# Optimization experiments

Hardware: AMD Instinct MI355X
Metric: run time of the kernel (lower is better)

## Reference

```python
import jax, jax.numpy as jnp
import numpy as np

B, L, D, N_ITEMS = 512, 128, 512, 50000


def setup_inputs() -> dict:
    key = jax.random.key(0)
    ks = jax.random.split(key, 12)
    s = 1.0 / np.sqrt(D)
    x = jax.random.randint(ks[0], (B, L), 0, N_ITEMS)
    # cumulative event times (strictly increasing per sequence)
    t = jnp.cumsum(jax.random.uniform(ks[1], (B, L), dtype=jnp.float32), axis=1)
    # embedding table, xavier-ish, padding_idx=0 row zeroed
    emb = (jax.random.normal(ks[2], (N_ITEMS, D), dtype=jnp.float32) * s).at[0].set(0.0)
    # GRUCell params (torch layout: gates ordered r, z, n)
    W_ih = jax.random.uniform(ks[3], (3 * D, D), minval=-s, maxval=s, dtype=jnp.float32)
    W_hh = jax.random.uniform(ks[4], (3 * D, D), minval=-s, maxval=s, dtype=jnp.float32)
    b_ih = jax.random.uniform(ks[5], (3 * D,), minval=-s, maxval=s, dtype=jnp.float32)
    b_hh = jax.random.uniform(ks[6], (3 * D,), minval=-s, maxval=s, dtype=jnp.float32)
    # ODEFunc: 2-layer MLP f(h) = W2 @ tanh(W1 @ h + b1) + b2
    W1 = jax.random.normal(ks[7], (D, D), dtype=jnp.float32) * s
    b1 = jnp.zeros((D,), jnp.float32)
    W2 = jax.random.normal(ks[8], (D, D), dtype=jnp.float32) * s
    b2 = jnp.zeros((D,), jnp.float32)
    return dict(t=t, emb=emb, W_ih=W_ih, W_hh=W_hh, b_ih=b_ih, b_hh=b_hh,
                W1=W1, b1=b1, W2=W2, b2=b2, x=x)


def reference(t, emb, W_ih, W_hh, b_ih, b_hh, W1, b1, W2, b2, x):
    dtype = emb.dtype
    x_emb = emb[x]  # [B, L, D]
    # inter-event deltas, dt[:,0] = 0
    dt = jnp.concatenate([jnp.zeros_like(t[:, :1]), t[:, 1:] - t[:, :-1]], axis=1)
    mask = (x != 0).astype(dtype)[..., None]  # [B, L, 1]

    def f(h):  # ODE dynamics (autonomous MLP)
        return jnp.tanh(h @ W1.T + b1) @ W2.T + b2

    def rk4(h, dt_):  # dt_ : [B, 1]
        k1 = f(h)
        k2 = f(h + 0.5 * dt_ * k1)
        k3 = f(h + 0.5 * dt_ * k2)
        k4 = f(h + dt_ * k3)
        return h + (dt_ / 6.0) * (k1 + 2.0 * k2 + 2.0 * k3 + k4)

    def gru_cell(xi, h):  # torch GRUCell math, gate order r,z,n
        gi = xi @ W_ih.T + b_ih
        gh = h @ W_hh.T + b_hh
        ir, iz, inn = jnp.split(gi, 3, axis=-1)
        hr, hz, hn = jnp.split(gh, 3, axis=-1)
        r = jax.nn.sigmoid(ir + hr)
        z = jax.nn.sigmoid(iz + hz)
        n = jnp.tanh(inn + r * hn)
        return (1.0 - z) * n + z * h

    xs = (jnp.swapaxes(x_emb, 0, 1),            # [L, B, D]
          jnp.swapaxes(dt, 0, 1)[..., None],    # [L, B, 1]
          jnp.swapaxes(mask, 0, 1),             # [L, B, 1]
          jnp.arange(t.shape[1]))               # step index

    def step(h, inp):
        xi, dti, mi, i = inp
        dti_c = jnp.maximum(dti, 1e-6)
        h_ev = rk4(h, dti_c)
        h = jnp.where(i > 0, h_ev * mi + h * (1.0 - mi), h)
        h_new = gru_cell(xi, h)
        h = h_new * mi + h * (1.0 - mi)
        return h, None

    h0 = jnp.zeros((t.shape[0], emb.shape[1]), dtype)
    h, _ = jax.lax.scan(step, h0, xs)
    return h  # [B, D]
```

## Files before the change

kernel.cpp:

```cpp
#include <hip/hip_runtime.h>

#define L_SEQ 128
#define BATCH 512
#define DIM   512

typedef __attribute__((ext_vector_type(8))) short bf16x8;
typedef __attribute__((ext_vector_type(4))) float f32x4;
typedef unsigned short ushort_t;

#define MFMA16(a,b,c) __builtin_amdgcn_mfma_f32_16x16x32_bf16((a),(b),(c),0,0,0)

__device__ __forceinline__ ushort_t f2bf(float f) {
  union { float f; unsigned u; } v; v.f = f;
  unsigned u = v.u;
  unsigned r = (u + 0x7FFFu + ((u >> 16) & 1u)) >> 16;
  return (ushort_t)r;
}
__device__ __forceinline__ float bf2f(ushort_t b) {
  union { unsigned u; float f; } v; v.u = ((unsigned)b) << 16;
  return v.f;
}
__device__ __forceinline__ int aoff(int r, int k) {
  return (r << 10) + ((((k >> 3) ^ (r & 7)) << 4) | ((k & 7) << 1));
}
__device__ __forceinline__ float tanh_f(float x) {
  x = fminf(fmaxf(x, -15.f), 15.f);
  float e = __expf(2.f * x);
  return (e - 1.f) / (e + 1.f);
}
__device__ __forceinline__ float sigm_f(float x) {
  x = fminf(fmaxf(x, -30.f), 30.f);
  return 1.f / (1.f + __expf(-x));
}


__global__ __launch_bounds__(256) void prep_w(const float* __restrict__ W1,
                                              const float* __restrict__ W2,
                                              const float* __restrict__ Whh,
                                              const float* __restrict__ Wih,
                                              ushort_t* __restrict__ wsb) {
  unsigned idx = blockIdx.x * 256u + threadIdx.x;
  unsigned m  = idx >> 18;
  unsigned r  = idx & 262143u;
  unsigned s  = r >> 14;
  unsigned r1 = r & 16383u;
  unsigned w  = r1 >> 10;
  unsigned r2 = r1 & 1023u;
  unsigned g  = r2 >> 8;
  unsigned r3 = r2 & 255u;
  unsigned cc = r3 >> 3;
  unsigned j  = r3 & 7u;
  unsigned c  = w * 32u + cc;
  unsigned k  = s * 32u + g * 8u + j;
  float v;
  if (m == 0)      v = W1[c * 512u + k];
  else if (m == 1) v = W2[c * 512u + k];
  else if (m < 5)  v = Whh[((m - 2u) * 512u + c) * 512u + k];
  else             v = Wih[((m - 5u) * 512u + c) * 512u + k];
  wsb[idx] = f2bf(v);
}

__global__ __launch_bounds__(256) void gi_gemm(const float* __restrict__ emb,
                                               const int* __restrict__ x,
                                               const float* __restrict__ bih,
                                               const ushort_t* __restrict__ wsb,
                                               ushort_t* __restrict__ gib) {
  __shared__ __align__(16) unsigned char As[64 * 1024];
  const int tid = threadIdx.x;
  const int mb = blockIdx.x;
  const int nb = blockIdx.y;
  const int i = (mb * 64) >> 9;
  const int brow0 = (mb * 64) & 511;
  {
    int r = tid >> 2;
    int xv = x[(brow0 + r) * L_SEQ + i];
    const float4* er4 = (const float4*)(emb + (size_t)xv * DIM);
#pragma unroll
    for (int cc = 0; cc < 16; ++cc) {
      int c = (tid & 3) * 16 + cc;
      float4 fa = er4[c * 2], fb = er4[c * 2 + 1];
      union { ushort_t u[8]; bf16x8 v; } pk;
      pk.u[0] = f2bf(fa.x); pk.u[1] = f2bf(fa.y); pk.u[2] = f2bf(fa.z); pk.u[3] = f2bf(fa.w);
      pk.u[4] = f2bf(fb.x); pk.u[5] = f2bf(fb.y); pk.u[6] = f2bf(fb.z); pk.u[7] = f2bf(fb.w);
      *(bf16x8*)(As + aoff(r, c * 8)) = pk.v;
    }
  }
  __syncthreads();
  const int wave = tid >> 6, lane = tid & 63;
  const int lr = lane & 15, lg = lane >> 4;
  const int ncol0 = nb * 256 + wave * 64;
  const int gate = nb >> 1;
  const ushort_t* wimg = wsb + (5u + (unsigned)gate) * 262144u;
  int bofs[4];
#pragma unroll
  for (int nf = 0; nf < 4; ++nf) {
    int cg = (nb & 1) * 256 + wave * 64 + nf * 16 + lr;
    bofs[nf] = (cg >> 5) * 1024 + (cg & 31) * 8 + lg * 256;
  }
  f32x4 acc[4][4];
  f32x4 z = {0.f, 0.f, 0.f, 0.f};
#pragma unroll
  for (int mf = 0; mf < 4; ++mf)
#pragma unroll
    for (int nf = 0; nf < 4; ++nf) acc[mf][nf] = z;
#pragma unroll
  for (int kf = 0; kf < 16; ++kf) {
    bf16x8 a[4];
#pragma unroll
    for (int mf = 0; mf < 4; ++mf)
      a[mf] = *(const bf16x8*)(As + aoff((mf << 4) + lr, (kf << 5) + (lg << 3)));
#pragma unroll
    for (int nf = 0; nf < 4; ++nf) {
      bf16x8 b = *(const bf16x8*)(wimg + kf * 16384 + bofs[nf]);
#pragma unroll
      for (int mf = 0; mf < 4; ++mf) acc[mf][nf] = MFMA16(a[mf], b, acc[mf][nf]);
    }
  }
#pragma unroll
  for (int nf = 0; nf < 4; ++nf) {
    int col = ncol0 + (nf << 4) + lr;
    float bb = bih[col];
#pragma unroll
    for (int mf = 0; mf < 4; ++mf)
#pragma unroll
      for (int j = 0; j < 4; ++j) {
        int row = (mf << 4) + (lg << 2) + j;
        __builtin_nontemporal_store(f2bf(acc[mf][nf][j] + bb),
            gib + (size_t)(i * BATCH + brow0 + row) * 1536 + col);
      }
  }
}


__device__ __forceinline__ void barrier_nd() {
  asm volatile("s_waitcnt lgkmcnt(0)" ::: "memory");
  __builtin_amdgcn_s_barrier();
}

__device__ __forceinline__ void dma_slice(const ushort_t* __restrict__ wsb,
                                          int ip, int ij, int wave, int lane,
                                          unsigned char* dst) {
  unsigned moff = (ip < 8) ? ((unsigned)(ip & 1) << 18) : ((unsigned)(ip - 6) << 18);
  const ushort_t* src = wsb + moff + ((unsigned)ij << 14) + ((unsigned)wave << 10) + ((unsigned)lane << 3);
  __builtin_amdgcn_global_load_lds((const __attribute__((address_space(1))) unsigned int*)src,
                                   (__attribute__((address_space(3))) unsigned int*)dst, 16, 0, 0);
  __builtin_amdgcn_global_load_lds((const __attribute__((address_space(1))) unsigned int*)(src + 512),
                                   (__attribute__((address_space(3))) unsigned int*)(dst + 1024), 16, 0, 0);
}

__device__ __forceinline__ void phase_mm(const unsigned char* __restrict__ Aimg,
                                         unsigned char* __restrict__ wbw,
                                         const ushort_t* __restrict__ wsb,
                                         int wave, int lane,
                                         int& cslot, int& ip, int& ij, f32x4 acc[2]) {
  const int lr = lane & 15, lg = lane >> 4;
  f32x4 z = {0.f, 0.f, 0.f, 0.f};
  acc[0] = z; acc[1] = z;
#pragma unroll 2
  for (int kf = 0; kf < 16; ++kf) {
    asm volatile("s_waitcnt vmcnt(4)" ::: "memory");
    __builtin_amdgcn_sched_barrier(0);
    unsigned char* wb = wbw + cslot * 2048;
    bf16x8 a = *(const bf16x8*)(Aimg + (lr << 10) + ((((kf << 2) + lg) ^ (lr & 7)) << 4));
    bf16x8 p = *(const bf16x8*)(wb + (lg << 9) + (lr << 4));
    bf16x8 q = *(const bf16x8*)(wb + (lg << 9) + 256 + (lr << 4));
    asm volatile("s_waitcnt lgkmcnt(0)" ::: "memory");
    __builtin_amdgcn_sched_barrier(0);
    dma_slice(wsb, ip, ij, wave, lane, wb);
    if (++ij == 16) { ij = 0; if (++ip == 11) ip = 0; }
    cslot = (cslot == 2) ? 0 : cslot + 1;
    acc[0] = MFMA16(a, p, acc[0]);
    acc[1] = MFMA16(a, q, acc[1]);
  }
}

__global__ __launch_bounds__(1024, 4) void scan_kernel(
    const float* __restrict__ t, const int* __restrict__ x,
    const ushort_t* __restrict__ wsb,
    const float* __restrict__ b1g, const float* __restrict__ b2g,
    const float* __restrict__ bhhg,
    const ushort_t* __restrict__ gib, float* __restrict__ out) {
  extern __shared__ unsigned char smem[];
  unsigned char* WBUF = smem;
  unsigned char* S0   = smem + 98304;
  unsigned char* S1   = smem + 114688;
  float* b1s  = (float*)(smem + 131072);
  float* b2s  = (float*)(smem + 133120);
  float* bhhs = (float*)(smem + 135168);

  const int tid = threadIdx.x;
  const int wave = tid >> 6, lane = tid & 63;
  const int lr = lane & 15, lg = lane >> 4;
  const int n0 = wave * 32;
  const int b0 = blockIdx.x * 16;
  unsigned char* wbw = WBUF + wave * 6144;

  for (int q = tid; q < 512; q += 1024) { b1s[q] = b1g[q]; b2s[q] = b2g[q]; }
  for (int q = tid; q < 1536; q += 1024) bhhs[q] = bhhg[q];
  { bf16x8 zz = {0, 0, 0, 0, 0, 0, 0, 0}; *(bf16x8*)(S0 + tid * 16) = zz; }
  __syncthreads();

  float dtj[4], mj[4];
#pragma unroll
  for (int j = 0; j < 4; ++j) {
    int b = b0 + lg * 4 + j;
    mj[j] = (x[b * L_SEQ + 0] != 0) ? 1.f : 0.f;
    dtj[j] = 1e-6f;
  }
  ushort_t gv[3][2][4];
#pragma unroll
  for (int nf = 0; nf < 2; ++nf)
#pragma unroll
    for (int j = 0; j < 4; ++j) {
      const ushort_t* gp = gib + (size_t)(b0 + lg * 4 + j) * 1536 + n0 + nf * 16 + lr;
      gv[0][nf][j] = __builtin_nontemporal_load(gp);
      gv[1][nf][j] = __builtin_nontemporal_load(gp + 512);
      gv[2][nf][j] = __builtin_nontemporal_load(gp + 1024);
    }

  int cslot = 0, ip = 8, ij = 0;
#pragma unroll
  for (int k = 0; k < 3; ++k) { dma_slice(wsb, ip, ij, wave, lane, wbw + k * 2048); ++ij; }

  float h[2][4];
#pragma unroll
  for (int nf = 0; nf < 2; ++nf)
#pragma unroll
    for (int j = 0; j < 4; ++j) h[nf][j] = 0.f;

  for (int i = 0; i < L_SEQ; ++i) {
    barrier_nd();

    if (i > 0) {
      float ksum[2][4] = {};
      for (int s = 0; s < 4; ++s) {
        f32x4 a1[2];
        phase_mm(S0, wbw, wsb, wave, lane, cslot, ip, ij, a1);
#pragma unroll
        for (int nf = 0; nf < 2; ++nf) {
          int col = n0 + nf * 16 + lr;
          float bb = b1s[col];
#pragma unroll
          for (int j = 0; j < 4; ++j)
            *(ushort_t*)(S1 + aoff(lg * 4 + j, col)) = f2bf(tanh_f(a1[nf][j] + bb));
        }
        barrier_nd();
        f32x4 a2[2];
        phase_mm(S1, wbw, wsb, wave, lane, cslot, ip, ij, a2);
        const float wk = (s == 0 || s == 3) ? 1.f : 2.f;
        const float cs = (s < 2) ? 0.5f : 1.f;
#pragma unroll
        for (int nf = 0; nf < 2; ++nf) {
          int col = n0 + nf * 16 + lr;
          float bb = b2s[col];
#pragma unroll
          for (int j = 0; j < 4; ++j) {
            float kv = a2[nf][j] + bb;
            ksum[nf][j] += wk * kv;
            float nv;
            if (s < 3) {
              nv = h[nf][j] + cs * dtj[j] * kv;
            } else {
              float hev = h[nf][j] + dtj[j] * (1.f / 6.f) * ksum[nf][j];
              nv = (mj[j] > 0.5f) ? hev : h[nf][j];
              h[nf][j] = nv;
            }
            *(ushort_t*)(S0 + aoff(lg * 4 + j, col)) = f2bf(nv);
          }
        }
        barrier_nd();
      }
    }

    f32x4 gh0[2], gh1[2], gh2[2];
    phase_mm(S0, wbw, wsb, wave, lane, cslot, ip, ij, gh0);
    phase_mm(S0, wbw, wsb, wave, lane, cslot, ip, ij, gh1);
    phase_mm(S0, wbw, wsb, wave, lane, cslot, ip, ij, gh2);
    barrier_nd();

    int in_ = (i < L_SEQ - 1) ? i + 1 : i;
    float dtn[4], mn[4];
#pragma unroll
    for (int j = 0; j < 4; ++j) {
      int b = b0 + lg * 4 + j;
      mn[j] = (x[b * L_SEQ + in_] != 0) ? 1.f : 0.f;
      dtn[j] = fmaxf(t[b * L_SEQ + in_] - t[b * L_SEQ + in_ - 1], 1e-6f);
    }
    ushort_t gvn[3][2][4];
#pragma unroll
    for (int nf = 0; nf < 2; ++nf)
#pragma unroll
      for (int j = 0; j < 4; ++j) {
        const ushort_t* gp = gib + (size_t)(in_ * BATCH + b0 + lg * 4 + j) * 1536 + n0 + nf * 16 + lr;
        gvn[0][nf][j] = __builtin_nontemporal_load(gp);
        gvn[1][nf][j] = __builtin_nontemporal_load(gp + 512);
        gvn[2][nf][j] = __builtin_nontemporal_load(gp + 1024);
      }

#pragma unroll
    for (int nf = 0; nf < 2; ++nf) {
      int col = n0 + nf * 16 + lr;
      float br = bhhs[col], bz = bhhs[col + 512], bn = bhhs[col + 1024];
#pragma unroll
      for (int j = 0; j < 4; ++j) {
        float rr = sigm_f(bf2f(gv[0][nf][j]) + gh0[nf][j] + br);
        float zz = sigm_f(bf2f(gv[1][nf][j]) + gh1[nf][j] + bz);
        float nn = tanh_f(bf2f(gv[2][nf][j]) + rr * (gh2[nf][j] + bn));
        float hnew = (1.f - zz) * nn + zz * h[nf][j];
        float hv = (mj[j] > 0.5f) ? hnew : h[nf][j];
        h[nf][j] = hv;
        *(ushort_t*)(S0 + aoff(lg * 4 + j, col)) = f2bf(hv);
      }
    }
#pragma unroll
    for (int j = 0; j < 4; ++j) { dtj[j] = dtn[j]; mj[j] = mn[j]; }
#pragma unroll
    for (int g = 0; g < 3; ++g)
#pragma unroll
      for (int nf = 0; nf < 2; ++nf)
#pragma unroll
        for (int j = 0; j < 4; ++j) gv[g][nf][j] = gvn[g][nf][j];
  }

  asm volatile("s_waitcnt vmcnt(0)" ::: "memory");
#pragma unroll
  for (int nf = 0; nf < 2; ++nf) {
    int col = n0 + nf * 16 + lr;
#pragma unroll
    for (int j = 0; j < 4; ++j) {
      int b = b0 + lg * 4 + j;
      out[(size_t)b * DIM + col] = h[nf][j];
    }
  }
}

extern "C" void kernel_launch(void* const* d_in, const int* in_sizes, int n_in,
                              void* d_out, int out_size, void* d_ws, size_t ws_size,
                              hipStream_t stream) {
  const float* t_   = (const float*)d_in[0];
  const float* emb  = (const float*)d_in[1];
  const float* Wih  = (const float*)d_in[2];
  const float* Whh  = (const float*)d_in[3];
  const float* bih  = (const float*)d_in[4];
  const float* bhh  = (const float*)d_in[5];
  const float* W1   = (const float*)d_in[6];
  const float* b1   = (const float*)d_in[7];
  const float* W2   = (const float*)d_in[8];
  const float* b2   = (const float*)d_in[9];
  const int*   x    = (const int*)d_in[10];
  float* out = (float*)d_out;
  (void)b2; (void)in_sizes; (void)n_in; (void)out_size; (void)ws_size;

  ushort_t* wsb = (ushort_t*)d_ws;
  ushort_t* gib = wsb + 2097152;

  (void)hipFuncSetAttribute((const void*)scan_kernel,
                            hipFuncAttributeMaxDynamicSharedMemorySize, 141312);

  hipLaunchKernelGGL(prep_w, dim3(8192), dim3(256), 0, stream, W1, W2, Whh, Wih, wsb);
  hipLaunchKernelGGL(gi_gemm, dim3(1024, 6), dim3(256), 0, stream, emb, x, bih, wsb, gib);
  hipLaunchKernelGGL(scan_kernel, dim3(32), dim3(1024), 141312, stream,
                     t_, x, wsb, b1, b2, bhh, gib, out);
}
```

Baseline: 7.696 ms.

## Split each batch group across two blocks exchanging hidden halves via global flags

The scan kernel now runs 64 blocks of 512 threads instead of 32 blocks of 1024. Each pair of blocks owns one batch group and computes half of the output columns each. At every matmul phase the two blocks swap their halves of the activation through global memory, guarded by atomic flag counters and spin-waits, and the final output buffer serves as the exchange scratch. Weights are streamed straight into registers with inline-asm global loads instead of the LDS DMA ring, and the weight image is re-laid out in column halves. The aim is to put twice as many CUs on the latency-bound recurrence, at the cost of a cross-block handshake on every phase.

```diff
diff --git a/kernel.cpp b/kernel.cpp
--- a/kernel.cpp
+++ b/kernel.cpp
@@ -31,6 +31,10 @@
 __device__ __forceinline__ float sigm_f(float x) {
   x = fminf(fmaxf(x, -30.f), 30.f);
   return 1.f / (1.f + __expf(-x));
+}
+__device__ __forceinline__ void barrier_nd() {
+  asm volatile("s_waitcnt lgkmcnt(0)" ::: "memory");
+  __builtin_amdgcn_s_barrier();
 }
 
 
@@ -42,15 +46,16 @@
   unsigned idx = blockIdx.x * 256u + threadIdx.x;
   unsigned m  = idx >> 18;
   unsigned r  = idx & 262143u;
-  unsigned s  = r >> 14;
-  unsigned r1 = r & 16383u;
+  unsigned hf = r >> 17;  r &= 131071u;
+  unsigned s  = r >> 13;
+  unsigned r1 = r & 8191u;
   unsigned w  = r1 >> 10;
   unsigned r2 = r1 & 1023u;
   unsigned g  = r2 >> 8;
   unsigned r3 = r2 & 255u;
   unsigned cc = r3 >> 3;
   unsigned j  = r3 & 7u;
-  unsigned c  = w * 32u + cc;
+  unsigned c  = hf * 256u + w * 32u + cc;
   unsigned k  = s * 32u + g * 8u + j;
   float v;
   if (m == 0)      v = W1[c * 512u + k];
@@ -95,7 +100,8 @@
 #pragma unroll
   for (int nf = 0; nf < 4; ++nf) {
     int cg = (nb & 1) * 256 + wave * 64 + nf * 16 + lr;
-    bofs[nf] = (cg >> 5) * 1024 + (cg & 31) * 8 + lg * 256;
+    int hfc = cg >> 8, chw = cg & 255;
+    bofs[nf] = hfc * 131072 + (chw >> 5) * 1024 + (chw & 31) * 8 + lg * 256;
   }
   f32x4 acc[4][4];
   f32x4 z = {0.f, 0.f, 0.f, 0.f};
@@ -111,7 +117,7 @@
       a[mf] = *(const bf16x8*)(As + aoff((mf << 4) + lr, (kf << 5) + (lg << 3)));
 #pragma unroll
     for (int nf = 0; nf < 4; ++nf) {
-      bf16x8 b = *(const bf16x8*)(wimg + kf * 16384 + bofs[nf]);
+      bf16x8 b = *(const bf16x8*)(wimg + kf * 8192 + bofs[nf]);
 #pragma unroll
       for (int mf = 0; mf < 4; ++mf) acc[mf][nf] = MFMA16(a[mf], b, acc[mf][nf]);
     }
@@ -132,73 +138,100 @@
 }
 
 
-__device__ __forceinline__ void barrier_nd() {
-  asm volatile("s_waitcnt lgkmcnt(0)" ::: "memory");
-  __builtin_amdgcn_s_barrier();
-}
-
-__device__ __forceinline__ void dma_slice(const ushort_t* __restrict__ wsb,
-                                          int ip, int ij, int wave, int lane,
-                                          unsigned char* dst) {
-  unsigned moff = (ip < 8) ? ((unsigned)(ip & 1) << 18) : ((unsigned)(ip - 6) << 18);
-  const ushort_t* src = wsb + moff + ((unsigned)ij << 14) + ((unsigned)wave << 10) + ((unsigned)lane << 3);
-  __builtin_amdgcn_global_load_lds((const __attribute__((address_space(1))) unsigned int*)src,
-                                   (__attribute__((address_space(3))) unsigned int*)dst, 16, 0, 0);
-  __builtin_amdgcn_global_load_lds((const __attribute__((address_space(1))) unsigned int*)(src + 512),
-                                   (__attribute__((address_space(3))) unsigned int*)(dst + 1024), 16, 0, 0);
-}
-
-__device__ __forceinline__ void phase_mm(const unsigned char* __restrict__ Aimg,
-                                         unsigned char* __restrict__ wbw,
-                                         const ushort_t* __restrict__ wsb,
-                                         int wave, int lane,
-                                         int& cslot, int& ip, int& ij, f32x4 acc[2]) {
-  const int lr = lane & 15, lg = lane >> 4;
-  f32x4 z = {0.f, 0.f, 0.f, 0.f};
-  acc[0] = z; acc[1] = z;
-#pragma unroll 2
-  for (int kf = 0; kf < 16; ++kf) {
-    asm volatile("s_waitcnt vmcnt(4)" ::: "memory");
-    __builtin_amdgcn_sched_barrier(0);
-    unsigned char* wb = wbw + cslot * 2048;
-    bf16x8 a = *(const bf16x8*)(Aimg + (lr << 10) + ((((kf << 2) + lg) ^ (lr & 7)) << 4));
-    bf16x8 p = *(const bf16x8*)(wb + (lg << 9) + (lr << 4));
-    bf16x8 q = *(const bf16x8*)(wb + (lg << 9) + 256 + (lr << 4));
-    asm volatile("s_waitcnt lgkmcnt(0)" ::: "memory");
-    __builtin_amdgcn_sched_barrier(0);
-    dma_slice(wsb, ip, ij, wave, lane, wb);
-    if (++ij == 16) { ij = 0; if (++ip == 11) ip = 0; }
-    cslot = (cslot == 2) ? 0 : cslot + 1;
-    acc[0] = MFMA16(a, p, acc[0]);
-    acc[1] = MFMA16(a, q, acc[1]);
-  }
-}
-
-__global__ __launch_bounds__(1024, 4) void scan_kernel(
+#define ISSUE16(BASE) do { \
+    _Pragma("unroll") \
+    for (int q_ = 0; q_ < 16; ++q_) { \
+      int s_ = (q_ < 8) ? (sb0 + q_) : (sb1 + q_ - 8); \
+      const ushort_t* a_ = (BASE) + (unsigned)s_ * 8192u; \
+      asm volatile("global_load_dwordx4 %0, %2, off\n\t" \
+                   "global_load_dwordx4 %1, %2, off offset:256" \
+                   : "=&v"(Rr[q_][0]), "=&v"(Rr[q_][1]) : "v"(a_) : "memory"); \
+    } } while (0)
+
+#define CONS1(IMG, Q, SS, VM) do { \
+    asm volatile("s_waitcnt vmcnt(" #VM ")" ::: "memory"); \
+    __builtin_amdgcn_sched_barrier(0); \
+    bf16x8 a_ = *(const bf16x8*)((IMG) + (lr << 10) + ((((SS) * 4 + lg) ^ (lr & 7)) << 4)); \
+    acc[0] = MFMA16(a_, Rr[Q][0], acc[0]); \
+    acc[1] = MFMA16(a_, Rr[Q][1], acc[1]); } while (0)
+
+#define CONS_LO(IMG) do { CONS1(IMG,0,sb0+0,30); CONS1(IMG,1,sb0+1,28); \
+    CONS1(IMG,2,sb0+2,26); CONS1(IMG,3,sb0+3,24); CONS1(IMG,4,sb0+4,22); \
+    CONS1(IMG,5,sb0+5,20); CONS1(IMG,6,sb0+6,18); CONS1(IMG,7,sb0+7,16); } while (0)
+#define CONS_HI(IMG) do { CONS1(IMG,8,sb1+0,14); CONS1(IMG,9,sb1+1,12); \
+    CONS1(IMG,10,sb1+2,10); CONS1(IMG,11,sb1+3,8); CONS1(IMG,12,sb1+4,6); \
+    CONS1(IMG,13,sb1+5,4); CONS1(IMG,14,sb1+6,2); CONS1(IMG,15,sb1+7,0); } while (0)
+
+#define HEAD() do { \
+    asm volatile("" :: "v"(o0), "v"(o1)); \
+    asm volatile("s_waitcnt vmcnt(0)" ::: "memory"); \
+    __syncthreads(); \
+    if (tid == 0) (void)__hip_atomic_fetch_add(myflag, 1u, __ATOMIC_RELAXED, __HIP_MEMORY_SCOPE_AGENT); \
+  } while (0)
+
+#define EXPORT(IMG) do { \
+    int row_ = tid >> 5, ch_ = tid & 31; \
+    union { unsigned long long u[2]; bf16x8 v; } pk_; \
+    pk_.v = *(const bf16x8*)((IMG) + (row_ << 10) + (((hf * 32 + ch_) ^ (row_ & 7)) << 4)); \
+    unsigned long long* d_ = xb + ((size_t)((g * 2 + (int)(pc & 1u)) * 2 + hf) * 1024) + tid * 2; \
+    o0 = __hip_atomic_exchange(d_,     pk_.u[0], __ATOMIC_RELAXED, __HIP_MEMORY_SCOPE_AGENT); \
+    o1 = __hip_atomic_exchange(d_ + 1, pk_.u[1], __ATOMIC_RELAXED, __HIP_MEMORY_SCOPE_AGENT); \
+  } while (0)
+
+#define IMPORT(IMG) do { \
+    if (tid == 0) { unsigned tgt_ = pc + 1u; \
+      while (__hip_atomic_load(pflag, __ATOMIC_RELAXED, __HIP_MEMORY_SCOPE_AGENT) < tgt_) \
+        __builtin_amdgcn_s_sleep(2); } \
+    __builtin_amdgcn_s_barrier(); \
+    int row_ = tid >> 5, ch_ = tid & 31; \
+    unsigned long long* s_ = xb + ((size_t)((g * 2 + (int)(pc & 1u)) * 2 + (hf ^ 1)) * 1024) + tid * 2; \
+    union { unsigned long long u[2]; bf16x8 v; } pk_; \
+    pk_.u[0] = __hip_atomic_fetch_add(s_,     0ull, __ATOMIC_RELAXED, __HIP_MEMORY_SCOPE_AGENT); \
+    pk_.u[1] = __hip_atomic_fetch_add(s_ + 1, 0ull, __ATOMIC_RELAXED, __HIP_MEMORY_SCOPE_AGENT); \
+    *(bf16x8*)((IMG) + (row_ << 10) + (((((hf ^ 1) * 32) + ch_) ^ (row_ & 7)) << 4)) = pk_.v; \
+    barrier_nd(); \
+  } while (0)
+
+__global__ __launch_bounds__(512, 2) void scan_kernel(
     const float* __restrict__ t, const int* __restrict__ x,
     const ushort_t* __restrict__ wsb,
     const float* __restrict__ b1g, const float* __restrict__ b2g,
     const float* __restrict__ bhhg,
-    const ushort_t* __restrict__ gib, float* __restrict__ out) {
-  extern __shared__ unsigned char smem[];
-  unsigned char* WBUF = smem;
-  unsigned char* S0   = smem + 98304;
-  unsigned char* S1   = smem + 114688;
-  float* b1s  = (float*)(smem + 131072);
-  float* b2s  = (float*)(smem + 133120);
-  float* bhhs = (float*)(smem + 135168);
+    const ushort_t* __restrict__ gib,
+    unsigned* __restrict__ flags,
+    float* __restrict__ out) {
+  __shared__ __align__(16) unsigned char S0[16 * 1024];
+  __shared__ __align__(16) unsigned char S1[16 * 1024];
+  __shared__ float b1s[512], b2s[512], bhhs[1536];
 
   const int tid = threadIdx.x;
   const int wave = tid >> 6, lane = tid & 63;
   const int lr = lane & 15, lg = lane >> 4;
-  const int n0 = wave * 32;
-  const int b0 = blockIdx.x * 16;
-  unsigned char* wbw = WBUF + wave * 6144;
-
-  for (int q = tid; q < 512; q += 1024) { b1s[q] = b1g[q]; b2s[q] = b2g[q]; }
-  for (int q = tid; q < 1536; q += 1024) bhhs[q] = bhhg[q];
-  { bf16x8 zz = {0, 0, 0, 0, 0, 0, 0, 0}; *(bf16x8*)(S0 + tid * 16) = zz; }
+  const int g = blockIdx.x >> 1, hf = blockIdx.x & 1;
+  const int b0 = g * 16;
+  const int colbase = hf * 256 + wave * 32;
+  const int sb0 = hf * 8, sb1 = (hf ^ 1) * 8;
+  unsigned* myflag = flags + (g * 2 + hf) * 16;
+  unsigned* pflag  = flags + (g * 2 + (hf ^ 1)) * 16;
+  unsigned long long* xb = (unsigned long long*)out;
+
+  const ushort_t* wl = wsb + (unsigned)hf * 131072u + (unsigned)wave * 1024u
+                           + (unsigned)lg * 256u + (unsigned)lr * 8u;
+  const ushort_t* base_w1 = wl;
+  const ushort_t* base_w2 = wl + 262144u;
+  const ushort_t* base_wr = wl + 2u * 262144u;
+  const ushort_t* base_wz = wl + 3u * 262144u;
+  const ushort_t* base_wn = wl + 4u * 262144u;
+
+  { int q = tid; b1s[q] = b1g[q]; b2s[q] = b2g[q]; }
+  for (int q = tid; q < 1536; q += 512) bhhs[q] = bhhg[q];
   __syncthreads();
+
+  float h[2][4];
+#pragma unroll
+  for (int nf = 0; nf < 2; ++nf)
+#pragma unroll
+    for (int j = 0; j < 4; ++j) h[nf][j] = 0.f;
 
   float dtj[4], mj[4];
 #pragma unroll
@@ -207,58 +240,42 @@
     mj[j] = (x[b * L_SEQ + 0] != 0) ? 1.f : 0.f;
     dtj[j] = 1e-6f;
   }
-  ushort_t gv[3][2][4];
-#pragma unroll
-  for (int nf = 0; nf < 2; ++nf)
-#pragma unroll
-    for (int j = 0; j < 4; ++j) {
-      const ushort_t* gp = gib + (size_t)(b0 + lg * 4 + j) * 1536 + n0 + nf * 16 + lr;
-      gv[0][nf][j] = __builtin_nontemporal_load(gp);
-      gv[1][nf][j] = __builtin_nontemporal_load(gp + 512);
-      gv[2][nf][j] = __builtin_nontemporal_load(gp + 1024);
-    }
-
-  int cslot = 0, ip = 8, ij = 0;
-#pragma unroll
-  for (int k = 0; k < 3; ++k) { dma_slice(wsb, ip, ij, wave, lane, wbw + k * 2048); ++ij; }
-
-  float h[2][4];
-#pragma unroll
-  for (int nf = 0; nf < 2; ++nf)
-#pragma unroll
-    for (int j = 0; j < 4; ++j) h[nf][j] = 0.f;
+
+  unsigned pc = 0;
+  unsigned long long o0 = 0, o1 = 0;
+  bf16x8 Rr[16][2];
+  f32x4 acc[2];
+  const f32x4 z4 = {0.f, 0.f, 0.f, 0.f};
 
   for (int i = 0; i < L_SEQ; ++i) {
-    barrier_nd();
-
     if (i > 0) {
       float ksum[2][4] = {};
-      for (int s = 0; s < 4; ++s) {
-        f32x4 a1[2];
-        phase_mm(S0, wbw, wsb, wave, lane, cslot, ip, ij, a1);
+#pragma unroll 1
+      for (int s4 = 0; s4 < 4; ++s4) {
+        HEAD(); ISSUE16(base_w1); acc[0] = z4; acc[1] = z4;
+        CONS_LO(S0); IMPORT(S0); CONS_HI(S0); ++pc;
 #pragma unroll
         for (int nf = 0; nf < 2; ++nf) {
-          int col = n0 + nf * 16 + lr;
-          float bb = b1s[col];
+          int col = colbase + nf * 16 + lr; float bb = b1s[col];
 #pragma unroll
           for (int j = 0; j < 4; ++j)
-            *(ushort_t*)(S1 + aoff(lg * 4 + j, col)) = f2bf(tanh_f(a1[nf][j] + bb));
+            *(ushort_t*)(S1 + aoff(lg * 4 + j, col)) = f2bf(tanh_f(acc[nf][j] + bb));
         }
         barrier_nd();
-        f32x4 a2[2];
-        phase_mm(S1, wbw, wsb, wave, lane, cslot, ip, ij, a2);
-        const float wk = (s == 0 || s == 3) ? 1.f : 2.f;
-        const float cs = (s < 2) ? 0.5f : 1.f;
+        EXPORT(S1);
+        HEAD(); ISSUE16(base_w2); acc[0] = z4; acc[1] = z4;
+        CONS_LO(S1); IMPORT(S1); CONS_HI(S1); ++pc;
+        const float wk = (s4 == 0 || s4 == 3) ? 1.f : 2.f;
+        const float cs = (s4 < 2) ? 0.5f : 1.f;
 #pragma unroll
         for (int nf = 0; nf < 2; ++nf) {
-          int col = n0 + nf * 16 + lr;
-          float bb = b2s[col];
+          int col = colbase + nf * 16 + lr; float bb = b2s[col];
 #pragma unroll
           for (int j = 0; j < 4; ++j) {
-            float kv = a2[nf][j] + bb;
+            float kv = acc[nf][j] + bb;
             ksum[nf][j] += wk * kv;
             float nv;
-            if (s < 3) {
+            if (s4 < 3) {
               nv = h[nf][j] + cs * dtj[j] * kv;
             } else {
               float hev = h[nf][j] + dtj[j] * (1.f / 6.f) * ksum[nf][j];
@@ -269,37 +286,53 @@
           }
         }
         barrier_nd();
+        EXPORT(S0);
       }
     }
 
+    ushort_t gv[3][2][4];
+#pragma unroll
+    for (int nf = 0; nf < 2; ++nf)
+#pragma unroll
+      for (int j = 0; j < 4; ++j) {
+        const ushort_t* gp = gib + (size_t)(i * BATCH + b0 + lg * 4 + j) * 1536
+                                 + colbase + nf * 16 + lr;
+        gv[0][nf][j] = __builtin_nontemporal_load(gp);
+        gv[1][nf][j] = __builtin_nontemporal_load(gp + 512);
+        gv[2][nf][j] = __builtin_nontemporal_load(gp + 1024);
+      }
+    float dtn[4], mn[4];
+    if (i < L_SEQ - 1) {
+#pragma unroll
+      for (int j = 0; j < 4; ++j) {
+        int b = b0 + lg * 4 + j;
+        mn[j] = (x[b * L_SEQ + i + 1] != 0) ? 1.f : 0.f;
+        dtn[j] = fmaxf(t[b * L_SEQ + i + 1] - t[b * L_SEQ + i], 1e-6f);
+      }
+    } else {
+#pragma unroll
+      for (int j = 0; j < 4; ++j) { mn[j] = mj[j]; dtn[j] = dtj[j]; }
+    }
+
     f32x4 gh0[2], gh1[2], gh2[2];
-    phase_mm(S0, wbw, wsb, wave, lane, cslot, ip, ij, gh0);
-    phase_mm(S0, wbw, wsb, wave, lane, cslot, ip, ij, gh1);
-    phase_mm(S0, wbw, wsb, wave, lane, cslot, ip, ij, gh2);
-    barrier_nd();
-
-    int in_ = (i < L_SEQ - 1) ? i + 1 : i;
-    float dtn[4], mn[4];
-#pragma unroll
-    for (int j = 0; j < 4; ++j) {
-      int b = b0 + lg * 4 + j;
-      mn[j] = (x[b * L_SEQ + in_] != 0) ? 1.f : 0.f;
-      dtn[j] = fmaxf(t[b * L_SEQ + in_] - t[b * L_SEQ + in_ - 1], 1e-6f);
-    }
-    ushort_t gvn[3][2][4];
-#pragma unroll
-    for (int nf = 0; nf < 2; ++nf)
-#pragma unroll
-      for (int j = 0; j < 4; ++j) {
-        const ushort_t* gp = gib + (size_t)(in_ * BATCH + b0 + lg * 4 + j) * 1536 + n0 + nf * 16 + lr;
-        gvn[0][nf][j] = __builtin_nontemporal_load(gp);
-        gvn[1][nf][j] = __builtin_nontemporal_load(gp + 512);
-        gvn[2][nf][j] = __builtin_nontemporal_load(gp + 1024);
-      }
+    if (i > 0) {
+      HEAD(); ISSUE16(base_wr); acc[0] = z4; acc[1] = z4;
+      CONS_LO(S0); IMPORT(S0); CONS_HI(S0); ++pc;
+      gh0[0] = acc[0]; gh0[1] = acc[1];
+      ISSUE16(base_wz); acc[0] = z4; acc[1] = z4;
+      CONS_LO(S0); CONS_HI(S0);
+      gh1[0] = acc[0]; gh1[1] = acc[1];
+      ISSUE16(base_wn); acc[0] = z4; acc[1] = z4;
+      CONS_LO(S0); CONS_HI(S0);
+      gh2[0] = acc[0]; gh2[1] = acc[1];
+      barrier_nd();
+    } else {
+      gh0[0] = z4; gh0[1] = z4; gh1[0] = z4; gh1[1] = z4; gh2[0] = z4; gh2[1] = z4;
+    }
 
 #pragma unroll
     for (int nf = 0; nf < 2; ++nf) {
-      int col = n0 + nf * 16 + lr;
+      int col = colbase + nf * 16 + lr;
       float br = bhhs[col], bz = bhhs[col + 512], bn = bhhs[col + 1024];
 #pragma unroll
       for (int j = 0; j < 4; ++j) {
@@ -312,20 +345,24 @@
         *(ushort_t*)(S0 + aoff(lg * 4 + j, col)) = f2bf(hv);
       }
     }
+    barrier_nd();
+    if (i < L_SEQ - 1) EXPORT(S0);
 #pragma unroll
     for (int j = 0; j < 4; ++j) { dtj[j] = dtn[j]; mj[j] = mn[j]; }
-#pragma unroll
-    for (int g = 0; g < 3; ++g)
-#pragma unroll
-      for (int nf = 0; nf < 2; ++nf)
-#pragma unroll
-        for (int j = 0; j < 4; ++j) gv[g][nf][j] = gvn[g][nf][j];
-  }
-
+  }
+
+  asm volatile("" :: "v"(o0), "v"(o1));
   asm volatile("s_waitcnt vmcnt(0)" ::: "memory");
+  __syncthreads();
+  if (tid == 0) {
+    (void)__hip_atomic_fetch_add(myflag, 1u, __ATOMIC_RELAXED, __HIP_MEMORY_SCOPE_AGENT);
+    while (__hip_atomic_load(pflag, __ATOMIC_RELAXED, __HIP_MEMORY_SCOPE_AGENT) < 1144u)
+      __builtin_amdgcn_s_sleep(2);
+  }
+  __builtin_amdgcn_s_barrier();
 #pragma unroll
   for (int nf = 0; nf < 2; ++nf) {
-    int col = n0 + nf * 16 + lr;
+    int col = colbase + nf * 16 + lr;
 #pragma unroll
     for (int j = 0; j < 4; ++j) {
       int b = b0 + lg * 4 + j;
@@ -353,12 +390,11 @@
 
   ushort_t* wsb = (ushort_t*)d_ws;
   ushort_t* gib = wsb + 2097152;
-
-  (void)hipFuncSetAttribute((const void*)scan_kernel,
-                            hipFuncAttributeMaxDynamicSharedMemorySize, 141312);
+  unsigned* flags = (unsigned*)((char*)d_ws + 2621440);
 
   hipLaunchKernelGGL(prep_w, dim3(8192), dim3(256), 0, stream, W1, W2, Whh, Wih, wsb);
   hipLaunchKernelGGL(gi_gemm, dim3(1024, 6), dim3(256), 0, stream, emb, x, bih, wsb, gib);
-  hipLaunchKernelGGL(scan_kernel, dim3(32), dim3(1024), 141312, stream,
-                     t_, x, wsb, b1, b2, bhh, gib, out);
-}
+  hipMemsetAsync((void*)flags, 0, 4096, stream);
+  hipLaunchKernelGGL(scan_kernel, dim3(64), dim3(512), 0, stream,
+                     t_, x, wsb, b1, b2, bhh, gib, flags, out);
+}
```

New measurement: 10.15 ms. +31.9%, slower.
